# Kernel tuning notes

Measured on AMD Instinct MI355X. Metric: run time of the kernel, lower is better.

Reference implementation:

```python
import jax, jax.numpy as jnp
import numpy as np

N = 50000
E = 800000
NUM_GRAPHS = 64
D_IN = 261
D_SAGE = 64
D_LIN = 32
N_SAGE_REST = 6
N_LIN_REST = 3
EPS = 1e-5


def _layernorm(x, g, b):
    mu = jnp.mean(x, axis=-1, keepdims=True)
    var = jnp.mean((x - mu) ** 2, axis=-1, keepdims=True)
    return (x - mu) * jax.lax.rsqrt(var + EPS) * g + b


def _sage_block(x, Wl, bl, Wr, g, b, src, dst, inv_deg, residual):
    # mean aggregation of neighbor (source) features onto targets
    msum = jax.ops.segment_sum(x[src], dst, num_segments=N)  # [N, d]
    mean = msum * inv_deg  # [N, d]
    f = mean @ Wl + bl + x @ Wr  # lin_l(aggr) + lin_r(x); lin_r has no bias
    f = jax.nn.gelu(f, approximate=False)
    f = _layernorm(f, g, b)
    if residual:
        f = f + x
    return f


def _lin_block(x, W, b, g, beta, residual):
    f = jax.nn.gelu(x @ W + b, approximate=False)
    f = _layernorm(f, g, beta)
    if residual:
        f = f + x
    return f


def setup_inputs() -> dict:
    key = jax.random.key(0)
    ks = jax.random.split(key, 24)
    x = jax.random.normal(ks[0], (N, D_IN), dtype=jnp.float32)
    edge_index = jax.random.randint(ks[1], (2, E), 0, N, dtype=jnp.int64)
    batch = jnp.sort(jax.random.randint(ks[2], (N,), 0, NUM_GRAPHS, dtype=jnp.int64))

    def glorot(k, shape):
        fan_in = shape[0]
        return jax.random.normal(k, shape, dtype=jnp.float32) / np.sqrt(fan_in)

    inp = {
        "x": x, "edge_index": edge_index, "batch": batch,
        # first SAGE block (261 -> 64, no residual)
        "Wl0": glorot(ks[3], (D_IN, D_SAGE)), "bl0": jnp.zeros((D_SAGE,), jnp.float32),
        "Wr0": glorot(ks[4], (D_IN, D_SAGE)),
        "g0": jnp.ones((D_SAGE,), jnp.float32), "beta0": jnp.zeros((D_SAGE,), jnp.float32),
        # 6 residual SAGE blocks (64 -> 64), stacked
        "Wl": glorot(ks[5], (N_SAGE_REST, D_SAGE, D_SAGE)),
        "bl": jnp.zeros((N_SAGE_REST, D_SAGE), jnp.float32),
        "Wr": glorot(ks[6], (N_SAGE_REST, D_SAGE, D_SAGE)),
        "g": jnp.ones((N_SAGE_REST, D_SAGE), jnp.float32),
        "beta": jnp.zeros((N_SAGE_REST, D_SAGE), jnp.float32),
        # MLP: first LinearBlock 64 -> 32 (no residual)
        "M0": glorot(ks[7], (D_SAGE, D_LIN)), "mb0": jnp.zeros((D_LIN,), jnp.float32),
        "mg0": jnp.ones((D_LIN,), jnp.float32), "mbeta0": jnp.zeros((D_LIN,), jnp.float32),
        # 3 residual LinearBlocks 32 -> 32, stacked
        "M": glorot(ks[8], (N_LIN_REST, D_LIN, D_LIN)),
        "mb": jnp.zeros((N_LIN_REST, D_LIN), jnp.float32),
        "mg": jnp.ones((N_LIN_REST, D_LIN), jnp.float32),
        "mbeta": jnp.zeros((N_LIN_REST, D_LIN), jnp.float32),
        # final Linear 32 -> 1
        "Wf": glorot(ks[9], (D_LIN, 1)), "bf": jnp.zeros((1,), jnp.float32),
    }
    return inp


def reference(x, edge_index, batch, Wl0, bl0, Wr0, g0, beta0, Wl, bl, Wr, g, beta,
              M0, mb0, mg0, mbeta0, M, mb, mg, mbeta, Wf, bf):
    src, dst = edge_index[0], edge_index[1]
    deg = jax.ops.segment_sum(jnp.ones((E,), x.dtype), dst, num_segments=N)
    inv_deg = (1.0 / jnp.maximum(deg, 1.0))[:, None]  # [N,1]

    h = _sage_block(x, Wl0, bl0, Wr0, g0, beta0, src, dst, inv_deg, residual=False)
    for i in range(N_SAGE_REST):
        h = _sage_block(h, Wl[i], bl[i], Wr[i], g[i], beta[i], src, dst, inv_deg, residual=True)

    pooled = jax.ops.segment_sum(h, batch, num_segments=NUM_GRAPHS)  # [G, 64]

    m = _lin_block(pooled, M0, mb0, mg0, mbeta0, residual=False)
    for i in range(N_LIN_REST):
        m = _lin_block(m, M[i], mb[i], mg[i], mbeta[i], residual=True)
    return m @ Wf + bf  # [G, 1]
```

## Files before the change

### kernel.cpp

```cpp
#include <hip/hip_runtime.h>
#include <hip/hip_bf16.h>
#include <math.h>

#define N_NODES 50000
#define N_EDGES 800000
#define NUM_GRAPHS 64
#define NPAD 50048
#define KPAD0 288
#define MAXDEG 64

#define GEMM0_GRID (NPAD / 64)
#define SCAT_GRID  ((N_EDGES + 255) / 256)
#define ZERO_GRID  ((N_NODES + 255) / 256)
#define PREPW_TOT  (128 * KPAD0 + 6 * 128 * 64)
#define PREPW_GRID ((PREPW_TOT + 255) / 256)

typedef __attribute__((ext_vector_type(8))) short short8;
typedef __attribute__((ext_vector_type(4))) float f32x4;

__device__ __forceinline__ float gelu_f(float v) {
    return 0.5f * v * (1.0f + erff(v * 0.70710678118654752440f));
}

__device__ __forceinline__ float half_sum32(float v) {
    v += __shfl_xor(v, 1); v += __shfl_xor(v, 2); v += __shfl_xor(v, 4);
    v += __shfl_xor(v, 8); v += __shfl_xor(v, 16);
    return v;
}

__device__ __forceinline__ float group_sum8(float v) {
    v += __shfl_xor(v, 1); v += __shfl_xor(v, 2); v += __shfl_xor(v, 4);
    return v;
}

__device__ __forceinline__ unsigned short f2bf(float f) {
    unsigned int u = __float_as_uint(f);
    unsigned int r = (u + 0x7fffu + ((u >> 16) & 1u)) >> 16;
    return (unsigned short)r;
}

__device__ __forceinline__ float bf_lo(unsigned int u) {
    return __uint_as_float(u << 16);
}
__device__ __forceinline__ float bf_hi(unsigned int u) {
    return __uint_as_float(u & 0xffff0000u);
}


__global__ void k_prep(int* __restrict__ deg, float* __restrict__ pooled,
                       const float* __restrict__ Wl0, const float* __restrict__ Wr0,
                       const float* __restrict__ Wl, const float* __restrict__ Wr,
                       unsigned short* __restrict__ Bt0, unsigned short* __restrict__ BtR) {
    const int blk = blockIdx.x, tid = threadIdx.x;
    if (blk < ZERO_GRID) {
        int i = blk * 256 + tid;
        if (i < N_NODES) deg[i] = 0;
        if (i < NUM_GRAPHS * 64) pooled[i] = 0.0f;
        return;
    }
    int idx = (blk - ZERO_GRID) * 256 + tid;
    const int n0 = 128 * KPAD0;
    if (idx < n0) {
        int j = idx / KPAD0, k = idx - j * KPAD0;
        float v = 0.0f;
        if (k < 261) v = (j < 64) ? Wl0[k * 64 + j] : Wr0[k * 64 + (j - 64)];
        Bt0[idx] = f2bf(v);
    } else if (idx < PREPW_TOT) {
        int r = idx - n0;
        int l = r >> 13;
        int rr = r & 8191;
        int j = rr >> 6, k = rr & 63;
        float v = (j < 64) ? Wl[l * 4096 + k * 64 + j] : Wr[l * 4096 + k * 64 + (j - 64)];
        BtR[r] = f2bf(v);
    }
}


__global__ __launch_bounds__(256) void k_front(
        const float* __restrict__ X, const unsigned short* __restrict__ Bt0,
        unsigned short* __restrict__ U, float* __restrict__ V,
        const int* __restrict__ src, const int* __restrict__ dst,
        int* __restrict__ deg, unsigned short* __restrict__ col64) {
    __shared__ __align__(16) unsigned short sA[64 * 32];
    __shared__ __align__(16) unsigned short sB[128 * 32];
    const int blk = blockIdx.x;
    const int tid = threadIdx.x;

    if (blk < GEMM0_GRID) {
        const int lane = tid & 63, wid = tid >> 6;
        const int l16 = lane & 15, quad = lane >> 4;
        const int m0 = blk * 64;
        f32x4 acc[8];
        #pragma unroll
        for (int j = 0; j < 8; ++j) { acc[j][0] = 0.f; acc[j][1] = 0.f; acc[j][2] = 0.f; acc[j][3] = 0.f; }
        const int arow = tid >> 2, apart = (tid & 3) << 3;
        const int node = m0 + arow;
        const int rowok = (node < N_NODES);
        for (int kc = 0; kc < KPAD0; kc += 32) {
            if (kc) __syncthreads();
            short8 av;
            #pragma unroll
            for (int j = 0; j < 8; ++j) {
                int kk = kc + apart + j;
                float val = (rowok && kk < 261) ? X[(size_t)node * 261 + kk] : 0.0f;
                av[j] = (short)f2bf(val);
            }
            *(short8*)&sA[arow * 32 + apart] = av;
            #pragma unroll
            for (int q = 0; q < 2; ++q) {
                int flat = q * 256 + tid;
                int br = flat >> 2, bp = (flat & 3) << 3;
                *(int4*)&sB[br * 32 + bp] = *(const int4*)&Bt0[(size_t)br * KPAD0 + kc + bp];
            }
            __syncthreads();
            short8 af = *(const short8*)&sA[(wid * 16 + l16) * 32 + quad * 8];
            #pragma unroll
            for (int j = 0; j < 8; ++j) {
                short8 bf = *(const short8*)&sB[(j * 16 + l16) * 32 + quad * 8];
                acc[j] = __builtin_amdgcn_mfma_f32_16x16x32_bf16(af, bf, acc[j], 0, 0, 0);
            }
        }
        const int rbase = m0 + wid * 16 + quad * 4;
        #pragma unroll
        for (int j = 0; j < 4; ++j)
            #pragma unroll
            for (int r = 0; r < 4; ++r)
                U[(size_t)(rbase + r) * 64 + j * 16 + l16] = f2bf(acc[j][r]);
        #pragma unroll
        for (int j = 4; j < 8; ++j)
            #pragma unroll
            for (int r = 0; r < 4; ++r)
                V[(size_t)(rbase + r) * 64 + (j - 4) * 16 + l16] = acc[j][r];
    } else {
        int i = (blk - GEMM0_GRID) * 256 + tid;
        if (i < N_EDGES) {
            int d = dst[i];
            int pos = atomicAdd(&deg[d], 1);
            if (pos < MAXDEG)
                __builtin_nontemporal_store((unsigned short)src[i], &col64[(d << 6) + pos]);
        }
    }
}


__global__ __launch_bounds__(256) void k_layer(
        const unsigned short* __restrict__ U_in, const float* __restrict__ V_in,
        unsigned short* __restrict__ h,
        const int* __restrict__ deg, const unsigned short* __restrict__ col64,
        const float* __restrict__ bias, const float* __restrict__ gam,
        const float* __restrict__ bet,
        const unsigned short* __restrict__ Bt_next,
        unsigned short* __restrict__ U_out, float* __restrict__ V_out,
        const int* __restrict__ batch, float* __restrict__ pooled,
        int residual, int have_gemm) {
    __shared__ __align__(16) unsigned short sA[2 * 64 * 32];
    __shared__ __align__(16) unsigned short sB[128 * 32];
    __shared__ float sPool[8 * 64];
    const int tid = threadIdx.x;
    const int lane = tid & 63, wid = tid >> 6;
    const int sub = lane >> 3, hl = lane & 7;
    const int base = lane & 56;
    const int m0 = blockIdx.x * 64;
    const uint4* __restrict__ Up = (const uint4*)U_in;
    const int is_last = (pooled != nullptr);

    int gmin = 0, span = 1;
    if (is_last) {
        gmin = batch[m0];
        int gmax = batch[min(m0 + 63, N_NODES - 1)];
        span = gmax - gmin + 1;
        for (int i = tid; i < 8 * 64; i += 256) sPool[i] = 0.0f;
        __syncthreads();
    }

    #pragma unroll
    for (int rep = 0; rep < 2; ++rep) {
        const int nl = rep * 32 + wid * 8 + sub;
        const int node = m0 + nl;
        const bool valid = (node < N_NODES);
        const int nd = valid ? node : 0;
        const int dg = valid ? deg[nd] : 0;
        const int cnt = min(dg, MAXDEG);
        uint4 cv = make_uint4(0u, 0u, 0u, 0u);
        if (valid) cv = *(const uint4*)&col64[((size_t)nd << 6) + hl * 8];
        float s0 = 0.f, s1 = 0.f, s2 = 0.f, s3 = 0.f, s4 = 0.f, s5 = 0.f, s6 = 0.f, s7 = 0.f;
        for (int b = 0; b * 8 < cnt; b += 2) {
            #pragma unroll
            for (int hh = 0; hh < 2; ++hh) {
                const int sl = base + b + hh;
                unsigned int p0 = (unsigned int)__shfl((int)cv.x, sl);
                unsigned int p1 = (unsigned int)__shfl((int)cv.y, sl);
                unsigned int p2 = (unsigned int)__shfl((int)cv.z, sl);
                unsigned int p3 = (unsigned int)__shfl((int)cv.w, sl);
                const int eb = (b + hh) * 8;
                int c[8];
                c[0] = (int)(p0 & 0xffffu); c[1] = (int)(p0 >> 16);
                c[2] = (int)(p1 & 0xffffu); c[3] = (int)(p1 >> 16);
                c[4] = (int)(p2 & 0xffffu); c[5] = (int)(p2 >> 16);
                c[6] = (int)(p3 & 0xffffu); c[7] = (int)(p3 >> 16);
                #pragma unroll
                for (int i = 0; i < 8; ++i) {
                    uint4 u = (eb + i < cnt) ? Up[(size_t)c[i] * 8 + hl] : make_uint4(0u, 0u, 0u, 0u);
                    s0 += bf_lo(u.x); s1 += bf_hi(u.x);
                    s2 += bf_lo(u.y); s3 += bf_hi(u.y);
                    s4 += bf_lo(u.z); s5 += bf_hi(u.z);
                    s6 += bf_lo(u.w); s7 += bf_hi(u.w);
                }
            }
        }
        const float id = 1.0f / fmaxf((float)dg, 1.0f);
        const float4 b0 = *(const float4*)&bias[8 * hl];
        const float4 b1 = *(const float4*)&bias[8 * hl + 4];
        float4 v0 = make_float4(0.f, 0.f, 0.f, 0.f), v1 = v0;
        if (valid) {
            v0 = *(const float4*)&V_in[(size_t)nd * 64 + 8 * hl];
            v1 = *(const float4*)&V_in[(size_t)nd * 64 + 8 * hl + 4];
        }
        float f0 = gelu_f(s0 * id + b0.x + v0.x);
        float f1 = gelu_f(s1 * id + b0.y + v0.y);
        float f2 = gelu_f(s2 * id + b0.z + v0.z);
        float f3 = gelu_f(s3 * id + b0.w + v0.w);
        float f4 = gelu_f(s4 * id + b1.x + v1.x);
        float f5 = gelu_f(s5 * id + b1.y + v1.y);
        float f6 = gelu_f(s6 * id + b1.z + v1.z);
        float f7 = gelu_f(s7 * id + b1.w + v1.w);
        float mu = group_sum8(((f0 + f1) + (f2 + f3)) + ((f4 + f5) + (f6 + f7))) * 0.015625f;
        float d0 = f0 - mu, d1 = f1 - mu, d2 = f2 - mu, d3 = f3 - mu;
        float d4 = f4 - mu, d5 = f5 - mu, d6 = f6 - mu, d7 = f7 - mu;
        float var = group_sum8(((d0 * d0 + d1 * d1) + (d2 * d2 + d3 * d3)) +
                               ((d4 * d4 + d5 * d5) + (d6 * d6 + d7 * d7))) * 0.015625f;
        float rs = rsqrtf(var + 1e-5f);
        const float4 g0v = *(const float4*)&gam[8 * hl];
        const float4 g1v = *(const float4*)&gam[8 * hl + 4];
        const float4 e0v = *(const float4*)&bet[8 * hl];
        const float4 e1v = *(const float4*)&bet[8 * hl + 4];
        f0 = d0 * rs * g0v.x + e0v.x;
        f1 = d1 * rs * g0v.y + e0v.y;
        f2 = d2 * rs * g0v.z + e0v.z;
        f3 = d3 * rs * g0v.w + e0v.w;
        f4 = d4 * rs * g1v.x + e1v.x;
        f5 = d5 * rs * g1v.y + e1v.y;
        f6 = d6 * rs * g1v.z + e1v.z;
        f7 = d7 * rs * g1v.w + e1v.w;
        if (residual && valid) {
            uint4 hu = ((const uint4*)h)[(size_t)nd * 8 + hl];
            f0 += bf_lo(hu.x); f1 += bf_hi(hu.x);
            f2 += bf_lo(hu.y); f3 += bf_hi(hu.y);
            f4 += bf_lo(hu.z); f5 += bf_hi(hu.z);
            f6 += bf_lo(hu.w); f7 += bf_hi(hu.w);
        }
        if (valid) {
            if (!is_last) {
                uint4 outw;
                outw.x = (unsigned int)f2bf(f0) | ((unsigned int)f2bf(f1) << 16);
                outw.y = (unsigned int)f2bf(f2) | ((unsigned int)f2bf(f3) << 16);
                outw.z = (unsigned int)f2bf(f4) | ((unsigned int)f2bf(f5) << 16);
                outw.w = (unsigned int)f2bf(f6) | ((unsigned int)f2bf(f7) << 16);
                ((uint4*)h)[(size_t)nd * 8 + hl] = outw;
                *(uint4*)&sA[(((hl >> 2) * 64 + nl) << 5) + (hl & 3) * 8] = outw;
            } else {
                int g = batch[nd];
                if (span <= 8) {
                    float* pp = &sPool[(g - gmin) * 64 + 8 * hl];
                    atomicAdd(&pp[0], f0); atomicAdd(&pp[1], f1);
                    atomicAdd(&pp[2], f2); atomicAdd(&pp[3], f3);
                    atomicAdd(&pp[4], f4); atomicAdd(&pp[5], f5);
                    atomicAdd(&pp[6], f6); atomicAdd(&pp[7], f7);
                } else {
                    float* pp = &pooled[(size_t)g * 64 + 8 * hl];
                    atomicAdd(&pp[0], f0); atomicAdd(&pp[1], f1);
                    atomicAdd(&pp[2], f2); atomicAdd(&pp[3], f3);
                    atomicAdd(&pp[4], f4); atomicAdd(&pp[5], f5);
                    atomicAdd(&pp[6], f6); atomicAdd(&pp[7], f7);
                }
            }
        } else if (!is_last) {
            uint4 z = make_uint4(0u, 0u, 0u, 0u);
            *(uint4*)&sA[(((hl >> 2) * 64 + nl) << 5) + (hl & 3) * 8] = z;
        }
    }

    if (is_last) {
        __syncthreads();
        if (span <= 8) {
            for (int i = tid; i < span * 64; i += 256)
                atomicAdd(&pooled[(size_t)(gmin + (i >> 6)) * 64 + (i & 63)], sPool[i]);
        }
        return;
    }
    if (!have_gemm) return;
    __syncthreads();

    const int l16 = lane & 15, quad = lane >> 4;
    f32x4 acc[8];
    #pragma unroll
    for (int j = 0; j < 8; ++j) { acc[j][0] = 0.f; acc[j][1] = 0.f; acc[j][2] = 0.f; acc[j][3] = 0.f; }
    for (int kc = 0; kc < 64; kc += 32) {
        if (kc) __syncthreads();
        #pragma unroll
        for (int q = 0; q < 2; ++q) {
            int flat = q * 256 + tid;
            int br = flat >> 2, bp = (flat & 3) << 3;
            *(int4*)&sB[br * 32 + bp] = *(const int4*)&Bt_next[(size_t)br * 64 + kc + bp];
        }
        __syncthreads();
        short8 af = *(const short8*)&sA[(((kc >> 5) * 64 + wid * 16 + l16) << 5) + quad * 8];
        #pragma unroll
        for (int j = 0; j < 8; ++j) {
            short8 bf = *(const short8*)&sB[(j * 16 + l16) * 32 + quad * 8];
            acc[j] = __builtin_amdgcn_mfma_f32_16x16x32_bf16(af, bf, acc[j], 0, 0, 0);
        }
    }
    const int rbase = m0 + wid * 16 + quad * 4;
    #pragma unroll
    for (int j = 0; j < 4; ++j)
        #pragma unroll
        for (int r = 0; r < 4; ++r)
            U_out[(size_t)(rbase + r) * 64 + j * 16 + l16] = f2bf(acc[j][r]);
    #pragma unroll
    for (int j = 4; j < 8; ++j)
        #pragma unroll
        for (int r = 0; r < 4; ++r)
            V_out[(size_t)(rbase + r) * 64 + (j - 4) * 16 + l16] = acc[j][r];
}


__global__ __launch_bounds__(1024) void k_head(const float* __restrict__ pooled,
                                               const float* __restrict__ M0, const float* __restrict__ mb0,
                                               const float* __restrict__ mg0, const float* __restrict__ mbeta0,
                                               const float* __restrict__ M, const float* __restrict__ mb,
                                               const float* __restrict__ mg, const float* __restrict__ mbeta,
                                               const float* __restrict__ Wf, const float* __restrict__ bf,
                                               float* __restrict__ out) {
    __shared__ float sP[64 * 64];
    __shared__ float sA[64 * 33];
    __shared__ float sB[64 * 33];
    const int tx = threadIdx.x, ty = threadIdx.y;
    const int tid = ty * 32 + tx;
    for (int i = tid; i < 64 * 64; i += 1024) sP[i] = pooled[i];
    __syncthreads();
    #pragma unroll
    for (int rr = 0; rr < 2; ++rr) {
        int r = ty + rr * 32;
        float a = mb0[tx];
        for (int k = 0; k < 64; ++k) a += sP[r * 64 + k] * M0[k * 32 + tx];
        a = gelu_f(a);
        float mu = half_sum32(a) * (1.0f / 32.0f);
        float d = a - mu;
        float var = half_sum32(d * d) * (1.0f / 32.0f);
        a = d * rsqrtf(var + 1e-5f) * mg0[tx] + mbeta0[tx];
        sA[r * 33 + tx] = a;
    }
    __syncthreads();
    float* cur = sA;
    float* nxt = sB;
    for (int L = 0; L < 3; ++L) {
        const float* Mi = M + L * 32 * 32;
        const float* mbi = mb + L * 32;
        const float* mgi = mg + L * 32;
        const float* mbetai = mbeta + L * 32;
        #pragma unroll
        for (int rr = 0; rr < 2; ++rr) {
            int r = ty + rr * 32;
            float a = mbi[tx];
            for (int k = 0; k < 32; ++k) a += cur[r * 33 + k] * Mi[k * 32 + tx];
            a = gelu_f(a);
            float mu = half_sum32(a) * (1.0f / 32.0f);
            float d = a - mu;
            float var = half_sum32(d * d) * (1.0f / 32.0f);
            a = d * rsqrtf(var + 1e-5f) * mgi[tx] + mbetai[tx] + cur[r * 33 + tx];
            nxt[r * 33 + tx] = a;
        }
        __syncthreads();
        float* t = cur; cur = nxt; nxt = t;
    }
    #pragma unroll
    for (int rr = 0; rr < 2; ++rr) {
        int r = ty + rr * 32;
        float p = cur[r * 33 + tx] * Wf[tx];
        p = half_sum32(p);
        if (tx == 0) out[r] = p + bf[0];
    }
}


extern "C" void kernel_launch(void* const* d_in, const int* in_sizes, int n_in,
                              void* d_out, int out_size, void* d_ws, size_t ws_size,
                              hipStream_t stream) {
    const int E = N_EDGES;

    const float* x    = (const float*)d_in[0];
    const int* eidx   = (const int*)d_in[1];
    const int* batch  = (const int*)d_in[2];
    const float* Wl0  = (const float*)d_in[3];
    const float* bl0  = (const float*)d_in[4];
    const float* Wr0  = (const float*)d_in[5];
    const float* g0   = (const float*)d_in[6];
    const float* bet0 = (const float*)d_in[7];
    const float* Wl   = (const float*)d_in[8];
    const float* bl   = (const float*)d_in[9];
    const float* Wr   = (const float*)d_in[10];
    const float* gR   = (const float*)d_in[11];
    const float* betR = (const float*)d_in[12];
    const float* M0   = (const float*)d_in[13];
    const float* mb0  = (const float*)d_in[14];
    const float* mg0  = (const float*)d_in[15];
    const float* mbe0 = (const float*)d_in[16];
    const float* M    = (const float*)d_in[17];
    const float* mb   = (const float*)d_in[18];
    const float* mg   = (const float*)d_in[19];
    const float* mbe  = (const float*)d_in[20];
    const float* Wf   = (const float*)d_in[21];
    const float* bf   = (const float*)d_in[22];

    const int* src = eidx;
    const int* dst = eidx + E;

    char* p = (char*)d_ws;
    auto alloc = [&](size_t bytes) -> void* {
        void* q = (void*)p;
        p += (bytes + 255) & ~(size_t)255;
        return q;
    };
    int*   deg    = (int*)alloc((size_t)N_NODES * 4);
    unsigned short* col64 = (unsigned short*)alloc((size_t)N_NODES * MAXDEG * 2);
    unsigned short* Bt0 = (unsigned short*)alloc((size_t)128 * KPAD0 * 2);
    unsigned short* BtR = (unsigned short*)alloc((size_t)6 * 128 * 64 * 2);
    unsigned short* Ua  = (unsigned short*)alloc((size_t)NPAD * 64 * 2);
    unsigned short* Ub  = (unsigned short*)alloc((size_t)NPAD * 64 * 2);
    float* Va   = (float*)alloc((size_t)NPAD * 64 * 4);
    float* Vb   = (float*)alloc((size_t)NPAD * 64 * 4);
    unsigned short* hbuf = (unsigned short*)alloc((size_t)NPAD * 64 * 2);
    float* pooled = (float*)alloc((size_t)NUM_GRAPHS * 64 * 4);

    k_prep<<<ZERO_GRID + PREPW_GRID, 256, 0, stream>>>(deg, pooled, Wl0, Wr0, Wl, Wr, Bt0, BtR);

    k_front<<<GEMM0_GRID + SCAT_GRID, 256, 0, stream>>>(
        x, Bt0, Ua, Va, src, dst, deg, col64);

    unsigned short* Uin = Ua;  float* Vin = Va;
    unsigned short* Uout = Ub; float* Vout = Vb;
    for (int i = 0; i < 7; ++i) {
        const float* bias = (i == 0) ? bl0  : bl  + (size_t)(i - 1) * 64;
        const float* gam  = (i == 0) ? g0   : gR  + (size_t)(i - 1) * 64;
        const float* bet  = (i == 0) ? bet0 : betR + (size_t)(i - 1) * 64;
        const int have_gemm = (i < 6);
        float* pool_arg = (i == 6) ? pooled : nullptr;
        k_layer<<<GEMM0_GRID, 256, 0, stream>>>(
            Uin, Vin, hbuf, deg, col64, bias, gam, bet,
            have_gemm ? (BtR + (size_t)i * 128 * 64) : BtR,
            Uout, Vout, batch, pool_arg, (i > 0) ? 1 : 0, have_gemm);
        unsigned short* tu = Uin; Uin = Uout; Uout = tu;
        float* tv = Vin; Vin = Vout; Vout = tv;
    }

    k_head<<<1, dim3(32, 32), 0, stream>>>(pooled, M0, mb0, mg0, mbe0, M, mb, mg, mbe, Wf, bf, (float*)d_out);
}
```

Baseline: 413.8 us.

## Sort nodes by degree within each tile to balance gather work across waves

Adds a small bitonic-sort kernel that orders the 64 nodes of each tile by in-degree and stores a per-tile permutation. The layer kernel then pairs the lowest-degree node of one rep with the highest-degree node of the other, so each 8-lane group does a more even total amount of neighbour gathering and waves diverge less. It also swaps the nontemporal store in the edge scatter for a plain store. The cost is one extra kernel launch and a byte lookup per node in every layer. The permutation changes which lanes handle which rows, so any later code that relies on that row mapping must use the permuted index.

```diff
diff --git a/kernel.cpp b/kernel.cpp
--- a/kernel.cpp
+++ b/kernel.cpp
@@ -136,10 +136,33 @@
         if (i < N_EDGES) {
             int d = dst[i];
             int pos = atomicAdd(&deg[d], 1);
-            if (pos < MAXDEG)
-                __builtin_nontemporal_store((unsigned short)src[i], &col64[(d << 6) + pos]);
-        }
-    }
+            if (pos < MAXDEG) col64[(d << 6) + pos] = (unsigned short)src[i];
+        }
+    }
+}
+
+
+__global__ __launch_bounds__(64) void k_sortperm(const int* __restrict__ deg,
+                                                 unsigned char* __restrict__ perm) {
+    __shared__ int sk[64];
+    const int t = threadIdx.x;
+    const int m0 = blockIdx.x * 64;
+    const int node = m0 + t;
+    int d = (node < N_NODES) ? deg[node] : 0;
+    sk[t] = (d << 6) | t;
+    __syncthreads();
+    for (int k = 2; k <= 64; k <<= 1) {
+        for (int j = k >> 1; j > 0; j >>= 1) {
+            int ixj = t ^ j;
+            if (ixj > t) {
+                int a = sk[t], b = sk[ixj];
+                bool up = ((t & k) == 0);
+                if ((a > b) == up) { sk[t] = b; sk[ixj] = a; }
+            }
+            __syncthreads();
+        }
+    }
+    perm[m0 + t] = (unsigned char)(sk[t] & 63);
 }
 
 
@@ -147,6 +170,7 @@
         const unsigned short* __restrict__ U_in, const float* __restrict__ V_in,
         unsigned short* __restrict__ h,
         const int* __restrict__ deg, const unsigned short* __restrict__ col64,
+        const unsigned char* __restrict__ perm,
         const float* __restrict__ bias, const float* __restrict__ gam,
         const float* __restrict__ bet,
         const unsigned short* __restrict__ Bt_next,
@@ -173,9 +197,12 @@
         __syncthreads();
     }
 
+    const int idx0 = wid * 8 + sub;
+
     #pragma unroll
     for (int rep = 0; rep < 2; ++rep) {
-        const int nl = rep * 32 + wid * 8 + sub;
+        const int rank = (rep == 0) ? idx0 : (63 - idx0);
+        const int nl = perm[m0 + rank];
         const int node = m0 + nl;
         const bool valid = (node < N_NODES);
         const int nd = valid ? node : 0;
@@ -424,6 +451,7 @@
     };
     int*   deg    = (int*)alloc((size_t)N_NODES * 4);
     unsigned short* col64 = (unsigned short*)alloc((size_t)N_NODES * MAXDEG * 2);
+    unsigned char* perm = (unsigned char*)alloc((size_t)NPAD);
     unsigned short* Bt0 = (unsigned short*)alloc((size_t)128 * KPAD0 * 2);
     unsigned short* BtR = (unsigned short*)alloc((size_t)6 * 128 * 64 * 2);
     unsigned short* Ua  = (unsigned short*)alloc((size_t)NPAD * 64 * 2);
@@ -437,6 +465,8 @@
 
     k_front<<<GEMM0_GRID + SCAT_GRID, 256, 0, stream>>>(
         x, Bt0, Ua, Va, src, dst, deg, col64);
+
+    k_sortperm<<<GEMM0_GRID, 64, 0, stream>>>(deg, perm);
 
     unsigned short* Uin = Ua;  float* Vin = Va;
     unsigned short* Uout = Ub; float* Vout = Vb;
@@ -447,7 +477,7 @@
         const int have_gemm = (i < 6);
         float* pool_arg = (i == 6) ? pooled : nullptr;
         k_layer<<<GEMM0_GRID, 256, 0, stream>>>(
-            Uin, Vin, hbuf, deg, col64, bias, gam, bet,
+            Uin, Vin, hbuf, deg, col64, perm, bias, gam, bet,
             have_gemm ? (BtR + (size_t)i * 128 * 64) : BtR,
             Uout, Vout, batch, pool_arg, (i > 0) ? 1 : 0, have_gemm);
         unsigned short* tu = Uin; Uin = Uout; Uout = tu;
```

Result: no change. 409.3 us (-1.1%).
